# Optimization experiments

Hardware: AMD Instinct MI355X
Metric: run time of the kernel (lower is better)

## Reference

```python
import jax, jax.numpy as jnp
import numpy as np

D_MODEL = 512
H = 8
D_K = D_MODEL // H


def setup_inputs() -> dict:
    key = jax.random.key(0)
    ks = jax.random.split(key, 11)
    B, S = 2, 2048
    scale = 1.0 / np.sqrt(D_MODEL)
    return {
        "q": jax.random.normal(ks[0], (B, S, D_MODEL), jnp.float32),
        "v": jax.random.normal(ks[1], (B, S, D_MODEL), jnp.float32),
        "k": jax.random.normal(ks[2], (B, S, D_MODEL), jnp.float32),
        "w_q": jax.random.normal(ks[3], (D_MODEL, D_MODEL), jnp.float32) * scale,
        "b_q": jnp.zeros((D_MODEL,), jnp.float32),
        "w_k": jax.random.normal(ks[4], (D_MODEL, D_MODEL), jnp.float32) * scale,
        "b_k": jnp.zeros((D_MODEL,), jnp.float32),
        "w_v": jax.random.normal(ks[5], (D_MODEL, D_MODEL), jnp.float32) * scale,
        "b_v": jnp.zeros((D_MODEL,), jnp.float32),
        "w_o": jax.random.normal(ks[6], (D_MODEL, D_MODEL), jnp.float32) * scale,
        "b_o": jnp.zeros((D_MODEL,), jnp.float32),
    }


def reference(q, v, k, w_q, b_q, w_k, b_k, w_v, b_v, w_o, b_o):
    B, S, _ = q.shape
    # projections (nn.Linear: x @ W.T + b)
    query = q @ w_q.T + b_q
    key_t = k @ w_k.T + b_k
    value = v @ w_v.T + b_v
    # split heads: [B, S, H, D_K] -> [B, H, S, D_K]
    query = query.reshape(B, S, H, D_K).transpose(0, 2, 1, 3)
    key_t = key_t.reshape(B, S, H, D_K).transpose(0, 2, 1, 3)
    value = value.reshape(B, S, H, D_K).transpose(0, 2, 1, 3)
    # unfused attention: full [B, H, S, S] score matrix
    scores = jnp.einsum("bhqd,bhkd->bhqk", query, key_t) / jnp.sqrt(
        jnp.asarray(D_K, query.dtype)
    )
    attn = jax.nn.softmax(scores, axis=-1)  # dropout inactive in eval
    x = jnp.einsum("bhqk,bhkd->bhqd", attn, value)
    # merge heads and output projection
    x = x.transpose(0, 2, 1, 3).reshape(B, S, D_MODEL)
    return x @ w_o.T + b_o
```

## Files before the change

### kernel.cpp

```cpp
#include <hip/hip_runtime.h>
#include <hip/hip_bf16.h>


typedef __attribute__((ext_vector_type(8))) short short8;
typedef __attribute__((ext_vector_type(4))) short short4v;
typedef __attribute__((ext_vector_type(4))) float f32x4;
typedef __attribute__((ext_vector_type(2))) unsigned int uint2v;

#define DM 512
#define SEQ 2048
#define NROW 4096
#define LOG2E 1.44269504088896341f
#define MFMA(a, b, c) __builtin_amdgcn_mfma_f32_16x16x32_bf16(a, b, c, 0, 0, 0)
#define FENCE() __asm__ __volatile__("" ::: "memory")

#if __has_builtin(__builtin_amdgcn_exp2f)
#define EXP2(x) __builtin_amdgcn_exp2f(x)
#else
#define EXP2(x) exp2f(x)
#endif

__device__ __forceinline__ float bf_bits2f(short s) {
    unsigned int u = ((unsigned int)(unsigned short)s) << 16;
    return __builtin_bit_cast(float, u);
}
__device__ __forceinline__ short f2bf_r(float f) {
    unsigned int u = __builtin_bit_cast(unsigned int, f) + 0x8000u;
    return (short)(u >> 16);
}
__device__ __forceinline__ unsigned int pack_bf16(float lo, float hi) {
    unsigned int ul = __builtin_bit_cast(unsigned int, lo) + 0x8000u;
    unsigned int uh = __builtin_bit_cast(unsigned int, hi) + 0x8000u;
    return __builtin_amdgcn_perm(uh, ul, 0x07060302u);
}

__device__ __forceinline__ void gload_lds16(const void* src, void* lds_dst) {
    __builtin_amdgcn_global_load_lds(
        (const __attribute__((address_space(1))) unsigned int*)src,
        (__attribute__((address_space(3))) unsigned int*)lds_dst, 16, 0, 0);
}

template <int ROWS, int NW>
__device__ __forceinline__ void stage_tile(const short* __restrict__ gsrc, size_t gstride,
                                           short* lds, int wave, int lane) {
    constexpr int ISSUES = ROWS * 8 / (64 * NW);
    #pragma unroll
    for (int i = 0; i < ISSUES; i++) {
        const int blk = i * NW + wave;
        const int g = blk * 64 + lane;
        const int row = g >> 3;
        const int cb = (g & 7) ^ (row & 7);
        gload_lds16(gsrc + (size_t)row * gstride + cb * 8, lds + (size_t)blk * 512);
    }
}

__device__ __forceinline__ bool detect_f32(const unsigned int* __restrict__ q, int* cnt_lds) {
    if (threadIdx.x == 0) *cnt_lds = 0;
    __syncthreads();
    int local = 0;
    for (int i = threadIdx.x; i < 1024; i += blockDim.x) {
        unsigned int lo = q[i] & 0x7FFFu;
        if (lo >= 0x3000u && lo < 0x4400u) local++;
    }
    if (local) atomicAdd(cnt_lds, local);
    __syncthreads();
    return *cnt_lds < 512;
}

struct ConvArgs { const void* src[11]; short* dst[11]; int n[11]; };
__global__ void convert_all(ConvArgs a) {
    __shared__ int cnt;
    const bool f32m = detect_f32((const unsigned int*)a.src[0], &cnt);
    if (!f32m) return;
    const int tid = blockIdx.x * 256 + threadIdx.x;
    const int stride = gridDim.x * 256;
    for (int s = 0; s < 11; s++) {
        const float4* sp = (const float4*)a.src[s];
        short4v* dp = (short4v*)a.dst[s];
        const int n4 = a.n[s] >> 2;
        for (int i = tid; i < n4; i += stride) {
            float4 v = sp[i];
            short4v o;
            o[0] = f2bf_r(v.x); o[1] = f2bf_r(v.y);
            o[2] = f2bf_r(v.z); o[3] = f2bf_r(v.w);
            dp[i] = o;
        }
    }
}

template <int MT>
__device__ __forceinline__ void gemm_core(const short* __restrict__ A,
                                          const short* __restrict__ W,
                                          int m0, int n0, short* Alds, short* Blds,
                                          int wave, int lane, f32x4 (&acc)[MT / 64][4]) {
    const int rc = lane & 15, quad = lane >> 4;
    const short* Ag = A + (size_t)m0 * DM;
    const short* Bg = W + (size_t)n0 * DM;
    constexpr int ABUF = MT * 64, BBUF = 64 * 64;
    constexpr int INFLIGHT = MT * 8 / 256 + 2;
    constexpr int NITER = DM / 64;

    stage_tile<MT, 4>(Ag, DM, Alds, wave, lane);
    stage_tile<64, 4>(Bg, DM, Blds, wave, lane);

    for (int i = 0; i < NITER; i++) {
        const int cur = i & 1;
        const short* Ac = Alds + cur * ABUF;
        const short* Bc = Blds + cur * BBUF;
        if (i + 1 < NITER) {
            stage_tile<MT, 4>(Ag + (i + 1) * 64, DM, Alds + (cur ^ 1) * ABUF, wave, lane);
            stage_tile<64, 4>(Bg + (i + 1) * 64, DM, Blds + (cur ^ 1) * BBUF, wave, lane);
            __builtin_amdgcn_s_waitcnt(0x3F70 | INFLIGHT);
        } else {
            __builtin_amdgcn_s_waitcnt(0x3F70);
        }
        FENCE();
        __builtin_amdgcn_s_barrier();
        FENCE();
        #pragma unroll
        for (int h = 0; h < 2; h++) {
            short8 bf[4];
            #pragma unroll
            for (int nt = 0; nt < 4; nt++) {
                const int br = nt * 16 + rc;
                bf[nt] = *(const short8*)&Bc[br * 64 + (((quad + 4 * h) ^ (br & 7)) * 8)];
            }
            #pragma unroll
            for (int ms = 0; ms < MT / 64; ms++) {
                const int ar = wave * (MT / 4) + ms * 16 + rc;
                short8 af = *(const short8*)&Ac[ar * 64 + (((quad + 4 * h) ^ (ar & 7)) * 8)];
                #pragma unroll
                for (int nt = 0; nt < 4; nt++)
                    acc[ms][nt] = MFMA(af, bf[nt], acc[ms][nt]);
            }
        }
        FENCE();
        __builtin_amdgcn_s_barrier();
        FENCE();
    }
}

struct QKVArgs {
    const short* Araw[3]; const short* Wraw[3]; const short* Braw[3];
    const short* Acv[3];  const short* Wcv[3];  const short* Bcv[3];
    short* Cq; short* Ck; short* Cv;
    const unsigned int* qraw;
};
__global__ __launch_bounds__(256, 3) void qkv_gemm(QKVArgs args) {
    __shared__ __align__(16) short Alds[2][128 * 64];
    __shared__ __align__(16) short Blds[2][64 * 64];
    __shared__ int cnt;
    const bool f32m = detect_f32(args.qraw, &cnt);
    const int z = blockIdx.z;
    const short* A    = f32m ? args.Acv[z] : args.Araw[z];
    const short* W    = f32m ? args.Wcv[z] : args.Wraw[z];
    const short* bias = f32m ? args.Bcv[z] : args.Braw[z];
    const int wave = threadIdx.x >> 6, lane = threadIdx.x & 63;
    const int rc = lane & 15, quad = lane >> 4;
    const int m0 = blockIdx.x * 128, n0 = blockIdx.y * 64;

    f32x4 acc[2][4] = {};
    gemm_core<128>(A, W, m0, n0, &Alds[0][0], &Blds[0][0], wave, lane, acc);

    if (z == 2) {
        const int hh = n0 >> 6;
        #pragma unroll
        for (int ms = 0; ms < 2; ms++) {
            const int mw = m0 + wave * 32 + ms * 16;
            const int b = mw >> 11, sb = (mw & 2047) + quad * 4;
            #pragma unroll
            for (int nt = 0; nt < 4; nt++) {
                const int d = nt * 16 + rc;
                const float bv = bf_bits2f(bias[n0 + d]);
                short4v pk;
                #pragma unroll
                for (int r = 0; r < 4; r++) pk[r] = f2bf_r(acc[ms][nt][r] + bv);
                *(short4v*)(args.Cv + ((size_t)((b * 8 + hh) * 64 + d)) * SEQ + sb) = pk;
            }
        }
    } else {
        short* C = (z == 0) ? args.Cq : args.Ck;
        const float sc = (z == 0) ? (0.125f * LOG2E) : 1.0f;
        #pragma unroll
        for (int ms = 0; ms < 2; ms++) {
            const int mw = m0 + wave * 32 + ms * 16;
            #pragma unroll
            for (int nt = 0; nt < 4; nt++) {
                const int col = n0 + nt * 16 + rc;
                const float bv = bf_bits2f(bias[col]);
                #pragma unroll
                for (int r = 0; r < 4; r++)
                    C[(size_t)(mw + quad * 4 + r) * DM + col] = f2bf_r((acc[ms][nt][r] + bv) * sc);
            }
        }
    }
}

__global__ __launch_bounds__(256, 4) void out_gemm(
    const short* __restrict__ A, const short* __restrict__ Wraw,
    const short* __restrict__ Wcv, const short* __restrict__ Braw,
    const short* __restrict__ Bcv, void* __restrict__ Cout,
    const unsigned int* __restrict__ qraw) {
    __shared__ __align__(16) short Alds[2][64 * 64];
    __shared__ __align__(16) short Blds[2][64 * 64];
    __shared__ int cnt;
    const bool f32m = detect_f32(qraw, &cnt);
    const short* W    = f32m ? Wcv : Wraw;
    const short* bias = f32m ? Bcv : Braw;
    const int wave = threadIdx.x >> 6, lane = threadIdx.x & 63;
    const int rc = lane & 15, quad = lane >> 4;
    const int m0 = blockIdx.x * 64, n0 = blockIdx.y * 64;
    f32x4 acc[1][4] = {};
    gemm_core<64>(A, W, m0, n0, &Alds[0][0], &Blds[0][0], wave, lane, acc);
    const int mw = m0 + wave * 16;
    #pragma unroll
    for (int nt = 0; nt < 4; nt++) {
        const int col = n0 + nt * 16 + rc;
        const float bv = bf_bits2f(bias[col]);
        #pragma unroll
        for (int r = 0; r < 4; r++) {
            const size_t idx = (size_t)(mw + quad * 4 + r) * DM + col;
            const float val = acc[0][nt][r] + bv;
            if (f32m) ((float*)Cout)[idx] = val;
            else      ((short*)Cout)[idx] = f2bf_r(val);
        }
    }
}

__global__ __launch_bounds__(256, 2) void attn_kernel(
    const short* __restrict__ Q, const short* __restrict__ K,
    const short* __restrict__ Vt, float* __restrict__ Opart,
    float* __restrict__ Lpart)
{
    __shared__ __align__(16) short Klds[3][64 * 64];
    __shared__ __align__(16) short Vlds[3][64 * 64];
    __shared__ __align__(16) short Plds[4][32 * 72];

    const int wave = threadIdx.x >> 6, lane = threadIdx.x & 63;
    const int rc = lane & 15, quad = lane >> 4;
    const int bh = blockIdx.y, z = blockIdx.z;
    const size_t baseQ = (size_t)(bh >> 3) * SEQ * DM + (size_t)(bh & 7) * 64;
    const short* Qb = Q + baseQ;
    const short* Kb = K + baseQ + (size_t)(z * 1024) * DM;
    const short* Vb = Vt + (size_t)bh * 64 * SEQ + z * 1024;
    const int q0 = blockIdx.x * 128 + wave * 32;

    short8 qa[2][2];
    #pragma unroll
    for (int ms = 0; ms < 2; ms++)
        #pragma unroll
        for (int h = 0; h < 2; h++)
            qa[ms][h] = *(const short8*)(Qb + (size_t)(q0 + ms * 16 + rc) * DM + h * 32 + quad * 8);

    short8 ones;
    #pragma unroll
    for (int j = 0; j < 8; j++) ones[j] = (short)0x3F80;

    f32x4 o[2][4] = {};
    f32x4 lsum[2] = {};
    short* Pw = &Plds[wave][0];

    int koff[4][2], voff[4][2];
    #pragma unroll
    for (int kt = 0; kt < 4; kt++) {
        const int row = rc * 4 + kt;
        #pragma unroll
        for (int h = 0; h < 2; h++)
            koff[kt][h] = row * 64 + (((quad + 4 * h) ^ (row & 7)) * 8);
    }
    #pragma unroll
    for (int dt = 0; dt < 4; dt++) {
        const int row = dt * 16 + rc;
        #pragma unroll
        for (int h = 0; h < 2; h++)
            voff[dt][h] = row * 64 + (((quad + 4 * h) ^ (row & 7)) * 8);
    }

    stage_tile<64, 4>(Kb, DM, &Klds[0][0], wave, lane);
    stage_tile<64, 4>(Vb, SEQ, &Vlds[0][0], wave, lane);
    stage_tile<64, 4>(Kb + (size_t)64 * DM, DM, &Klds[1][0], wave, lane);
    stage_tile<64, 4>(Vb + 64, SEQ, &Vlds[1][0], wave, lane);

    auto body = [&](int it, int cur) {
        if (it < 14) {
            const int k0n = (it + 2) * 64;
            const int nb = (cur + 2) % 3;
            stage_tile<64, 4>(Kb + (size_t)k0n * DM, DM, &Klds[nb][0], wave, lane);
            stage_tile<64, 4>(Vb + k0n, SEQ, &Vlds[nb][0], wave, lane);
            __builtin_amdgcn_s_waitcnt(0x3F78);
        } else if (it == 14) {
            __builtin_amdgcn_s_waitcnt(0x3F74);
        } else {
            __builtin_amdgcn_s_waitcnt(0x3F70);
        }
        FENCE();
        __builtin_amdgcn_s_barrier();
        FENCE();

        const short* Kt = &Klds[cur][0];
        const short* Vl = &Vlds[cur][0];

        short8 kf[4][2];
        #pragma unroll
        for (int kt = 0; kt < 4; kt++)
            #pragma unroll
            for (int h = 0; h < 2; h++)
                kf[kt][h] = *(const short8*)&Kt[koff[kt][h]];
        f32x4 s[2][4];
        #pragma unroll
        for (int ms = 0; ms < 2; ms++)
            #pragma unroll
            for (int kt = 0; kt < 4; kt++) {
                f32x4 t = {};
                t = MFMA(qa[ms][0], kf[kt][0], t);
                t = MFMA(qa[ms][1], kf[kt][1], t);
                s[ms][kt] = t;
            }
        #pragma unroll
        for (int ms = 0; ms < 2; ms++)
            #pragma unroll
            for (int r = 0; r < 4; r++) {
                uint2v pk;
                pk[0] = pack_bf16(EXP2(s[ms][0][r]), EXP2(s[ms][1][r]));
                pk[1] = pack_bf16(EXP2(s[ms][2][r]), EXP2(s[ms][3][r]));
                *(uint2v*)(&Pw[(ms * 16 + quad * 4 + r) * 72 + rc * 4]) = pk;
            }
        __builtin_amdgcn_s_waitcnt(0xC07F);
        short8 pa[2][2];
        #pragma unroll
        for (int ms = 0; ms < 2; ms++)
            #pragma unroll
            for (int h = 0; h < 2; h++)
                pa[ms][h] = *(const short8*)(&Pw[(ms * 16 + rc) * 72 + h * 32 + quad * 8]);
        #pragma unroll
        for (int ms = 0; ms < 2; ms++) {
            lsum[ms] = MFMA(pa[ms][0], ones, lsum[ms]);
            lsum[ms] = MFMA(pa[ms][1], ones, lsum[ms]);
        }
        #pragma unroll
        for (int dt = 0; dt < 4; dt++) {
            short8 v0 = *(const short8*)&Vl[voff[dt][0]];
            short8 v1 = *(const short8*)&Vl[voff[dt][1]];
            #pragma unroll
            for (int ms = 0; ms < 2; ms++) {
                o[ms][dt] = MFMA(pa[ms][0], v0, o[ms][dt]);
                o[ms][dt] = MFMA(pa[ms][1], v1, o[ms][dt]);
            }
        }
        FENCE();
        __builtin_amdgcn_s_barrier();
        FENCE();
    };

    for (int itp = 0; itp < 15; itp += 3) {
        body(itp, 0);
        body(itp + 1, 1);
        body(itp + 2, 2);
    }
    body(15, 0);

    const size_t obase = ((size_t)(z * 16 + bh)) * SEQ;
    #pragma unroll
    for (int ms = 0; ms < 2; ms++) {
        const int qrow = q0 + ms * 16 + quad * 4;
        if (rc == 0) {
            #pragma unroll
            for (int r = 0; r < 4; r++)
                Lpart[obase + qrow + r] = lsum[ms][r];
        }
        #pragma unroll
        for (int dt = 0; dt < 4; dt++)
            #pragma unroll
            for (int r = 0; r < 4; r++)
                Opart[(obase + qrow + r) * 64 + dt * 16 + rc] = o[ms][dt][r];
    }
}

__global__ void attn_reduce(const float* __restrict__ Opart, const float* __restrict__ Lpart,
                            short* __restrict__ X) {
    const int idx = blockIdx.x * 256 + threadIdx.x;
    const int dq = idx & 15;
    const int bhq = idx >> 4;
    const int bh = bhq >> 11, q = bhq & 2047;
    const float4 o0 = ((const float4*)Opart)[(size_t)bhq * 16 + dq];
    const float4 o1 = ((const float4*)Opart)[(size_t)(bhq + 16 * SEQ) * 16 + dq];
    const float inv = 1.0f / (Lpart[bhq] + Lpart[bhq + 16 * SEQ]);
    short4v pk;
    pk[0] = f2bf_r((o0.x + o1.x) * inv);
    pk[1] = f2bf_r((o0.y + o1.y) * inv);
    pk[2] = f2bf_r((o0.z + o1.z) * inv);
    pk[3] = f2bf_r((o0.w + o1.w) * inv);
    const size_t row = (size_t)(bh >> 3) * SEQ + q;
    *(short4v*)(&X[row * DM + (bh & 7) * 64 + dq * 4]) = pk;
}

extern "C" void kernel_launch(void* const* d_in, const int* in_sizes, int n_in,
                              void* d_out, int out_size, void* d_ws, size_t ws_size,
                              hipStream_t stream) {
    char* ws = (char*)d_ws;
    const size_t SEQB = (size_t)NROW * DM * sizeof(short);
    const size_t WB   = (size_t)DM * DM * sizeof(short);
    const size_t BB   = (size_t)DM * sizeof(short);

    size_t off = 0;
    short* qc = (short*)(ws + off); off += SEQB;
    short* vc = (short*)(ws + off); off += SEQB;
    short* kc = (short*)(ws + off); off += SEQB;
    short* wq = (short*)(ws + off); off += WB;
    short* wk = (short*)(ws + off); off += WB;
    short* wv = (short*)(ws + off); off += WB;
    short* wo = (short*)(ws + off); off += WB;
    short* bq = (short*)(ws + off); off += BB;
    short* bk = (short*)(ws + off); off += BB;
    short* bv = (short*)(ws + off); off += BB;
    short* bo = (short*)(ws + off); off += BB;
    off = (off + 255) & ~(size_t)255;
    short* Qp  = (short*)(ws + off); off += SEQB;
    short* Kp  = (short*)(ws + off); off += SEQB;
    short* Vtp = (short*)(ws + off); off += SEQB;
    short* Xp  = (short*)(ws + off); off += SEQB;
    float* Opart = (float*)(ws + off); off += (size_t)2 * 16 * SEQ * 64 * sizeof(float);
    float* Lpart = (float*)(ws + off); off += (size_t)2 * 16 * SEQ * sizeof(float);

    ConvArgs ca;
    const void* srcs[11] = {d_in[0], d_in[1], d_in[2], d_in[3], d_in[5], d_in[7],
                            d_in[9], d_in[4], d_in[6], d_in[8], d_in[10]};
    short* dsts[11] = {qc, vc, kc, wq, wk, wv, wo, bq, bk, bv, bo};
    int ns[11] = {NROW * DM, NROW * DM, NROW * DM, DM * DM, DM * DM, DM * DM,
                  DM * DM, DM, DM, DM, DM};
    for (int i = 0; i < 11; i++) { ca.src[i] = srcs[i]; ca.dst[i] = dsts[i]; ca.n[i] = ns[i]; }
    convert_all<<<256, 256, 0, stream>>>(ca);

    QKVArgs qa;
    qa.Araw[0] = (const short*)d_in[0]; qa.Araw[1] = (const short*)d_in[2]; qa.Araw[2] = (const short*)d_in[1];
    qa.Wraw[0] = (const short*)d_in[3]; qa.Wraw[1] = (const short*)d_in[5]; qa.Wraw[2] = (const short*)d_in[7];
    qa.Braw[0] = (const short*)d_in[4]; qa.Braw[1] = (const short*)d_in[6]; qa.Braw[2] = (const short*)d_in[8];
    qa.Acv[0] = qc; qa.Acv[1] = kc; qa.Acv[2] = vc;
    qa.Wcv[0] = wq; qa.Wcv[1] = wk; qa.Wcv[2] = wv;
    qa.Bcv[0] = bq; qa.Bcv[1] = bk; qa.Bcv[2] = bv;
    qa.Cq = Qp; qa.Ck = Kp; qa.Cv = Vtp;
    qa.qraw = (const unsigned int*)d_in[0];
    qkv_gemm<<<dim3(NROW / 128, DM / 64, 3), 256, 0, stream>>>(qa);

    attn_kernel<<<dim3(SEQ / 128, 16, 2), 256, 0, stream>>>(Qp, Kp, Vtp, Opart, Lpart);
    attn_reduce<<<dim3(16 * SEQ * 16 / 256), 256, 0, stream>>>(Opart, Lpart, Xp);

    out_gemm<<<dim3(NROW / 64, DM / 64), 256, 0, stream>>>(
        Xp, (const short*)d_in[9], wo, (const short*)d_in[10], bo,
        d_out, (const unsigned int*)d_in[0]);
}
```

Before: 157.1 us.

## Triple-buffer GEMM LDS staging with one barrier per iteration and fix K swizzle

Projection GEMMs move from double to triple LDS buffering, prefetching two tiles ahead and issuing loads after a single barrier per k-step, which removes the trailing barrier. The attention loop is restructured the same way, with one barrier per iteration and prefetch issued after it. The K tile swizzle now uses row>>2 to match the rc-based read pattern and cut LDS bank conflicts. Occupancy bounds drop to 2 blocks per CU because the larger LDS footprint limits residency.

```diff
diff --git a/kernel.cpp b/kernel.cpp
--- a/kernel.cpp
+++ b/kernel.cpp
@@ -13,6 +13,9 @@
 #define LOG2E 1.44269504088896341f
 #define MFMA(a, b, c) __builtin_amdgcn_mfma_f32_16x16x32_bf16(a, b, c, 0, 0, 0)
 #define FENCE() __asm__ __volatile__("" ::: "memory")
+#define WAITVM(n) __builtin_amdgcn_s_waitcnt(0x3F70 | (n))
+#define WAITLGKM0() __builtin_amdgcn_s_waitcnt(0xC07F)
+#define BARRIER() do { FENCE(); __builtin_amdgcn_s_barrier(); FENCE(); } while (0)
 
 #if __has_builtin(__builtin_amdgcn_exp2f)
 #define EXP2(x) __builtin_amdgcn_exp2f(x)
@@ -40,7 +43,7 @@
         (__attribute__((address_space(3))) unsigned int*)lds_dst, 16, 0, 0);
 }
 
-template <int ROWS, int NW>
+template <int ROWS, int NW, int SH>
 __device__ __forceinline__ void stage_tile(const short* __restrict__ gsrc, size_t gstride,
                                            short* lds, int wave, int lane) {
     constexpr int ISSUES = ROWS * 8 / (64 * NW);
@@ -49,7 +52,7 @@
         const int blk = i * NW + wave;
         const int g = blk * 64 + lane;
         const int row = g >> 3;
-        const int cb = (g & 7) ^ (row & 7);
+        const int cb = (g & 7) ^ ((row >> SH) & 7);
         gload_lds16(gsrc + (size_t)row * gstride + cb * 8, lds + (size_t)blk * 512);
     }
 }
@@ -97,26 +100,26 @@
     const short* Ag = A + (size_t)m0 * DM;
     const short* Bg = W + (size_t)n0 * DM;
     constexpr int ABUF = MT * 64, BBUF = 64 * 64;
-    constexpr int INFLIGHT = MT * 8 / 256 + 2;
+    constexpr int IN = MT * 8 / 256 + 2;
     constexpr int NITER = DM / 64;
 
-    stage_tile<MT, 4>(Ag, DM, Alds, wave, lane);
-    stage_tile<64, 4>(Bg, DM, Blds, wave, lane);
-
+    stage_tile<MT, 4, 0>(Ag, DM, Alds, wave, lane);
+    stage_tile<64, 4, 0>(Bg, DM, Blds, wave, lane);
+    stage_tile<MT, 4, 0>(Ag + 64, DM, Alds + ABUF, wave, lane);
+    stage_tile<64, 4, 0>(Bg + 64, DM, Blds + BBUF, wave, lane);
+
+    #pragma unroll
     for (int i = 0; i < NITER; i++) {
-        const int cur = i & 1;
+        const int cur = i % 3;
+        if (i + 1 < NITER) WAITVM(IN); else WAITVM(0);
+        BARRIER();
+        if (i + 2 < NITER) {
+            const int nb = (i + 2) % 3;
+            stage_tile<MT, 4, 0>(Ag + (i + 2) * 64, DM, Alds + nb * ABUF, wave, lane);
+            stage_tile<64, 4, 0>(Bg + (i + 2) * 64, DM, Blds + nb * BBUF, wave, lane);
+        }
         const short* Ac = Alds + cur * ABUF;
         const short* Bc = Blds + cur * BBUF;
-        if (i + 1 < NITER) {
-            stage_tile<MT, 4>(Ag + (i + 1) * 64, DM, Alds + (cur ^ 1) * ABUF, wave, lane);
-            stage_tile<64, 4>(Bg + (i + 1) * 64, DM, Blds + (cur ^ 1) * BBUF, wave, lane);
-            __builtin_amdgcn_s_waitcnt(0x3F70 | INFLIGHT);
-        } else {
-            __builtin_amdgcn_s_waitcnt(0x3F70);
-        }
-        FENCE();
-        __builtin_amdgcn_s_barrier();
-        FENCE();
         #pragma unroll
         for (int h = 0; h < 2; h++) {
             short8 bf[4];
@@ -134,9 +137,6 @@
                     acc[ms][nt] = MFMA(af, bf[nt], acc[ms][nt]);
             }
         }
-        FENCE();
-        __builtin_amdgcn_s_barrier();
-        FENCE();
     }
 }
 
@@ -146,9 +146,9 @@
     short* Cq; short* Ck; short* Cv;
     const unsigned int* qraw;
 };
-__global__ __launch_bounds__(256, 3) void qkv_gemm(QKVArgs args) {
-    __shared__ __align__(16) short Alds[2][128 * 64];
-    __shared__ __align__(16) short Blds[2][64 * 64];
+__global__ __launch_bounds__(256, 2) void qkv_gemm(QKVArgs args) {
+    __shared__ __align__(16) short Alds[3][128 * 64];
+    __shared__ __align__(16) short Blds[3][64 * 64];
     __shared__ int cnt;
     const bool f32m = detect_f32(args.qraw, &cnt);
     const int z = blockIdx.z;
@@ -196,13 +196,13 @@
     }
 }
 
-__global__ __launch_bounds__(256, 4) void out_gemm(
+__global__ __launch_bounds__(256, 2) void out_gemm(
     const short* __restrict__ A, const short* __restrict__ Wraw,
     const short* __restrict__ Wcv, const short* __restrict__ Braw,
     const short* __restrict__ Bcv, void* __restrict__ Cout,
     const unsigned int* __restrict__ qraw) {
-    __shared__ __align__(16) short Alds[2][64 * 64];
-    __shared__ __align__(16) short Blds[2][64 * 64];
+    __shared__ __align__(16) short Alds[3][64 * 64];
+    __shared__ __align__(16) short Blds[3][64 * 64];
     __shared__ int cnt;
     const bool f32m = detect_f32(qraw, &cnt);
     const short* W    = f32m ? Wcv : Wraw;
@@ -266,7 +266,7 @@
         const int row = rc * 4 + kt;
         #pragma unroll
         for (int h = 0; h < 2; h++)
-            koff[kt][h] = row * 64 + (((quad + 4 * h) ^ (row & 7)) * 8);
+            koff[kt][h] = row * 64 + (((quad + 4 * h) ^ (rc & 7)) * 8);
     }
     #pragma unroll
     for (int dt = 0; dt < 4; dt++) {
@@ -276,27 +276,22 @@
             voff[dt][h] = row * 64 + (((quad + 4 * h) ^ (row & 7)) * 8);
     }
 
-    stage_tile<64, 4>(Kb, DM, &Klds[0][0], wave, lane);
-    stage_tile<64, 4>(Vb, SEQ, &Vlds[0][0], wave, lane);
-    stage_tile<64, 4>(Kb + (size_t)64 * DM, DM, &Klds[1][0], wave, lane);
-    stage_tile<64, 4>(Vb + 64, SEQ, &Vlds[1][0], wave, lane);
-
-    auto body = [&](int it, int cur) {
-        if (it < 14) {
+    stage_tile<64, 4, 2>(Kb, DM, &Klds[0][0], wave, lane);
+    stage_tile<64, 4, 0>(Vb, SEQ, &Vlds[0][0], wave, lane);
+    stage_tile<64, 4, 2>(Kb + (size_t)64 * DM, DM, &Klds[1][0], wave, lane);
+    stage_tile<64, 4, 0>(Vb + 64, SEQ, &Vlds[1][0], wave, lane);
+
+    #pragma unroll
+    for (int it = 0; it < 16; it++) {
+        const int cur = it % 3;
+        if (it + 1 < 16) WAITVM(4); else WAITVM(0);
+        BARRIER();
+        if (it + 2 < 16) {
             const int k0n = (it + 2) * 64;
-            const int nb = (cur + 2) % 3;
-            stage_tile<64, 4>(Kb + (size_t)k0n * DM, DM, &Klds[nb][0], wave, lane);
-            stage_tile<64, 4>(Vb + k0n, SEQ, &Vlds[nb][0], wave, lane);
-            __builtin_amdgcn_s_waitcnt(0x3F78);
-        } else if (it == 14) {
-            __builtin_amdgcn_s_waitcnt(0x3F74);
-        } else {
-            __builtin_amdgcn_s_waitcnt(0x3F70);
-        }
-        FENCE();
-        __builtin_amdgcn_s_barrier();
-        FENCE();
-
+            const int nb = (it + 2) % 3;
+            stage_tile<64, 4, 2>(Kb + (size_t)k0n * DM, DM, &Klds[nb][0], wave, lane);
+            stage_tile<64, 4, 0>(Vb + k0n, SEQ, &Vlds[nb][0], wave, lane);
+        }
         const short* Kt = &Klds[cur][0];
         const short* Vl = &Vlds[cur][0];
 
@@ -325,7 +320,7 @@
                 pk[1] = pack_bf16(EXP2(s[ms][2][r]), EXP2(s[ms][3][r]));
                 *(uint2v*)(&Pw[(ms * 16 + quad * 4 + r) * 72 + rc * 4]) = pk;
             }
-        __builtin_amdgcn_s_waitcnt(0xC07F);
+        WAITLGKM0();
         short8 pa[2][2];
         #pragma unroll
         for (int ms = 0; ms < 2; ms++)
@@ -347,17 +342,7 @@
                 o[ms][dt] = MFMA(pa[ms][1], v1, o[ms][dt]);
             }
         }
-        FENCE();
-        __builtin_amdgcn_s_barrier();
-        FENCE();
-    };
-
-    for (int itp = 0; itp < 15; itp += 3) {
-        body(itp, 0);
-        body(itp + 1, 1);
-        body(itp + 2, 2);
-    }
-    body(15, 0);
+    }
 
     const size_t obase = ((size_t)(z * 16 + bh)) * SEQ;
     #pragma unroll
```

Result: no change. 156.1 us (-0.6%).
